# Kernel optimization log

Hardware: AMD Instinct MI355X
Metric: run time of the kernel (lower is better)

## Reference

```python
import jax, jax.numpy as jnp
import numpy as np

NL, DM, DS, DC, EX = 4, 1024, 16, 4, 2
DI = EX * DM          # 2048 inner dim
DTR = DM // 16        # 64 dt_rank
HID, OUT = 2048, 1000
B, L = 2, 1024
EPS = 1e-5

def _ln(x, w, b):
    m = jnp.mean(x, -1, keepdims=True)
    v = jnp.var(x, -1, keepdims=True)
    return (x - m) / jnp.sqrt(v + EPS) * w + b

def _silu(x):
    return x * jax.nn.sigmoid(x)

def _dwconv(x, w, b):
    # x: (B,L,C), w: (C,K) depthwise causal conv
    K = w.shape[1]
    xp = jnp.pad(x, ((0, 0), (K - 1, 0), (0, 0)))
    kern = jnp.transpose(w)[:, None, :]  # (K,1,C)
    y = jax.lax.conv_general_dilated(xp, kern, (1,), 'VALID',
                                     dimension_numbers=('NLC', 'LIO', 'NLC'),
                                     feature_group_count=x.shape[-1])
    return y + b

def _selective_scan(xs_, dt, Bm, Cm, A, Dv):
    # xs_, dt: (B,L,DI); Bm, Cm: (B,L,DS); A: (DI,DS); Dv: (DI,)
    def step(h, inp):
        x_t, dt_t, B_t, C_t = inp  # (B,DI),(B,DI),(B,DS),(B,DS)
        dA = jnp.exp(dt_t[..., None] * A)                       # (B,DI,DS)
        h = dA * h + dt_t[..., None] * B_t[:, None, :] * x_t[..., None]
        return h, jnp.einsum('bdn,bn->bd', h, C_t)
    h0 = jnp.zeros((xs_.shape[0], A.shape[0], A.shape[1]), xs_.dtype)
    seq = tuple(jnp.swapaxes(t, 0, 1) for t in (xs_, dt, Bm, Cm))
    _, ys = jax.lax.scan(step, h0, seq)
    return jnp.swapaxes(ys, 0, 1) + xs_ * Dv

def _mamba_block(x, ipw, cw, cb, xpw, dpw, dpb, Alog, Dv, opw):
    xz = jnp.einsum('bld,ed->ble', x, ipw)          # (B,L,2*DI)
    xs_, z = jnp.split(xz, 2, -1)
    xs_ = _silu(_dwconv(xs_, cw, cb))
    xdbl = jnp.einsum('bld,ed->ble', xs_, xpw)      # (B,L,DTR+2*DS)
    dt, Bm, Cm = jnp.split(xdbl, [DTR, DTR + DS], -1)
    dt = jax.nn.softplus(jnp.einsum('blr,dr->bld', dt, dpw) + dpb)
    A = -jnp.exp(Alog)
    y = _selective_scan(xs_, dt, Bm, Cm, A, Dv)
    y = y * _silu(z)
    return jnp.einsum('bld,ed->ble', y, opw)

def setup_inputs() -> dict:
    key = jax.random.key(0)
    ks = jax.random.split(key, 16)
    s = 0.02
    return {
        'x': jax.random.normal(ks[0], (B, L, DM), jnp.float32),
        'ln_w': jnp.ones((NL, DM)), 'ln_b': jnp.zeros((NL, DM)),
        'in_proj_w': jax.random.normal(ks[1], (NL, 2 * DI, DM)) * s,
        'conv_w': jax.random.normal(ks[2], (NL, DI, DC)) * s,
        'conv_b': jnp.zeros((NL, DI)),
        'x_proj_w': jax.random.normal(ks[3], (NL, DTR + 2 * DS, DI)) * s,
        'dt_proj_w': jax.random.normal(ks[4], (NL, DI, DTR)) * s,
        'dt_proj_b': jax.random.uniform(ks[5], (NL, DI), minval=-4.0, maxval=-2.0),
        'A_log': jnp.log(jnp.broadcast_to(jnp.arange(1, DS + 1, dtype=jnp.float32), (NL, DI, DS)) + 0.0),
        'Dv': jnp.ones((NL, DI)),
        'out_proj_w': jax.random.normal(ks[6], (NL, DM, DI)) * s,
        'fn_w': jnp.ones((DM,)), 'fn_b': jnp.zeros((DM,)),
        'h1_w': jax.random.normal(ks[7], (HID, DM)) * s, 'h1_b': jnp.zeros((HID,)),
        'hln_w': jnp.ones((HID,)), 'hln_b': jnp.zeros((HID,)),
        'h2_w': jax.random.normal(ks[8], (OUT, HID)) * s, 'h2_b': jnp.zeros((OUT,)),
    }

def reference(x, ln_w, ln_b, in_proj_w, conv_w, conv_b, x_proj_w, dt_proj_w,
              dt_proj_b, A_log, Dv, out_proj_w, fn_w, fn_b,
              h1_w, h1_b, hln_w, hln_b, h2_w, h2_b):
    for i in range(NL):
        res = x
        xn = _ln(x, ln_w[i], ln_b[i])
        x = _mamba_block(xn, in_proj_w[i], conv_w[i], conv_b[i], x_proj_w[i],
                         dt_proj_w[i], dt_proj_b[i], A_log[i], Dv[i], out_proj_w[i]) + res
    x = _ln(x, fn_w, fn_b)
    last = x[:, -1, :]                               # (B, DM)
    h = jax.nn.gelu(_ln(last @ h1_w.T + h1_b, hln_w, hln_b), approximate=False)
    return h @ h2_w.T + h2_b                         # (B, OUT)
```

## Files before the change

### kernel.cpp

```cpp
#include <hip/hip_runtime.h>

typedef unsigned short u16;
using short8 = __attribute__((ext_vector_type(8))) short;
using f32x4  = __attribute__((ext_vector_type(4))) float;

#define NLAYER 4
#define DMODEL 1024
#define DSTATE 16
#define DINNER 2048
#define DTRANK 64
#define SEQL   1024
#define NBATCH 2
#define MTOK   2048
#define NCH    64
#define CLEN   16
#define XPK    16

__device__ __forceinline__ u16 f2bf(float f) {
  union { float f; unsigned int u; } cv; cv.f = f;
  return (u16)((cv.u + 0x7FFFu + ((cv.u >> 16) & 1u)) >> 16);
}
__device__ __forceinline__ float bf2f(u16 v) {
  union { unsigned int u; float f; } cv; cv.u = ((unsigned int)v) << 16; return cv.f;
}

__global__ __launch_bounds__(256) void f32_to_bf16_l(const float* __restrict__ src,
                                                     u16* __restrict__ dst, int nper) {
  int l = blockIdx.y;
  int i4 = (blockIdx.x * 256 + threadIdx.x) * 4;
  if (i4 >= nper) return;
  float4 v = *(const float4*)&src[(size_t)l * nper + i4];
  ushort4 o; o.x = f2bf(v.x); o.y = f2bf(v.y); o.z = f2bf(v.z); o.w = f2bf(v.w);
  *(ushort4*)&dst[(size_t)l * nper + i4] = o;
}

__global__ __launch_bounds__(256) void cvt_pad_xproj_l(const float* __restrict__ src,
                                                       u16* __restrict__ dst) {
  int l = blockIdx.y;
  int i4 = (blockIdx.x * 256 + threadIdx.x) * 4;
  int row = i4 >> 11, col = i4 & 2047;
  float4 v = make_float4(0.f, 0.f, 0.f, 0.f);
  if (row < 96) v = *(const float4*)&src[(size_t)l * 96 * 2048 + row * 2048 + col];
  ushort4 o; o.x = f2bf(v.x); o.y = f2bf(v.y); o.z = f2bf(v.z); o.w = f2bf(v.w);
  *(ushort4*)&dst[(size_t)l * 128 * 2048 + i4] = o;
}

__global__ __launch_bounds__(256) void ln_to_bf16_k(const float* __restrict__ X,
    const float* __restrict__ w, const float* __restrict__ b, u16* __restrict__ out) {
  int row = blockIdx.x, tid = threadIdx.x;
  const float* x = X + (size_t)row * 1024;
  float4 v = ((const float4*)x)[tid];
  float s = v.x + v.y + v.z + v.w;
  float q = v.x*v.x + v.y*v.y + v.z*v.z + v.w*v.w;
  for (int o = 32; o; o >>= 1) { s += __shfl_down(s, o); q += __shfl_down(q, o); }
  __shared__ float sb[4], qb[4];
  int wv = tid >> 6, lane = tid & 63;
  if (lane == 0) { sb[wv] = s; qb[wv] = q; }
  __syncthreads();
  s = sb[0] + sb[1] + sb[2] + sb[3];
  q = qb[0] + qb[1] + qb[2] + qb[3];
  float mean = s * (1.f / 1024.f);
  float var  = q * (1.f / 1024.f) - mean * mean;
  float rstd = rsqrtf(var + 1e-5f);
  float4 wv4 = ((const float4*)w)[tid];
  float4 bv4 = ((const float4*)b)[tid];
  ushort4 o4;
  o4.x = f2bf((v.x - mean) * rstd * wv4.x + bv4.x);
  o4.y = f2bf((v.y - mean) * rstd * wv4.y + bv4.y);
  o4.z = f2bf((v.z - mean) * rstd * wv4.z + bv4.z);
  o4.w = f2bf((v.w - mean) * rstd * wv4.w + bv4.w);
  ((ushort4*)(out + (size_t)row * 1024))[tid] = o4;
}

__device__ __forceinline__ void stage_tile(const u16* G, int ld, int row0, int k0,
                                           u16* S, int tid) {
  int w = tid >> 6;
#pragma unroll
  for (int j = 0; j < 2; ++j) {
    int t = tid + j * 256;
    int r = t >> 2;
    int c = (t & 3) << 3;
    const u16* g = G + (size_t)(row0 + r) * ld + (k0 + c);
    u16* s = S + w * 512 + j * 2048;
    __builtin_amdgcn_global_load_lds((const __attribute__((address_space(1))) void*)g,
                                     (__attribute__((address_space(3))) void*)s,
                                     16, 0, 0);
  }
}
__device__ __forceinline__ void stage512(const u16* G, int ld, int row0, int k0,
                                         u16* S, int tid) {
  int r = tid >> 2;
  int c = (tid & 3) << 3;
  const u16* g = G + (size_t)(row0 + r) * ld + (k0 + c);
  u16* s = S + (tid >> 6) * 512;
  __builtin_amdgcn_global_load_lds((const __attribute__((address_space(1))) void*)g,
                                   (__attribute__((address_space(3))) void*)s,
                                   16, 0, 0);
}

template<int EPI, int SWZ>
__global__ __launch_bounds__(512) void gemm_bt(const u16* __restrict__ A,
    const u16* __restrict__ Bw, float* __restrict__ C,
    int lda, int ldb, int ldc, int kchunk, int nbm, int zstride) {
  __shared__ u16 As[2][128 * 32];
  __shared__ u16 Bs[2][128 * 32];
  int tid = threadIdx.x;
  int bm, bn;
  if (SWZ) {
    int l = blockIdx.x;
    int xcd = l & 7;
    int idx = l >> 3;
    int bnr = (int)(gridDim.x >> 3) / nbm;
    bm = idx % nbm;
    bn = xcd * bnr + idx / nbm;
  } else {
    bm = blockIdx.x; bn = blockIdx.y;
  }
  int kb = blockIdx.z * kchunk, ke = kb + kchunk;
  int lane = tid & 63;
  int w = tid >> 6;
  int wr = (w >> 2) * 64;
  int wc = (w & 3) * 32;
  int fr = lane & 15;
  int kg = (lane >> 4) * 8;
  f32x4 acc[4][2] = {};
  int cur = 0;
  stage512(A, lda, bm * 128, kb, As[0], tid);
  stage512(Bw, ldb, bn * 128, kb, Bs[0], tid);
  __syncthreads();
  for (int k0 = kb; k0 < ke; k0 += 32) {
    int kn = k0 + 32;
    if (kn < ke) {
      stage512(A, lda, bm * 128, kn, As[cur ^ 1], tid);
      stage512(Bw, ldb, bn * 128, kn, Bs[cur ^ 1], tid);
    }
    short8 a[4], b[2];
#pragma unroll
    for (int mf = 0; mf < 4; ++mf)
      a[mf] = *(const short8*)&As[cur][(wr + mf * 16 + fr) * 32 + kg];
#pragma unroll
    for (int nf = 0; nf < 2; ++nf)
      b[nf] = *(const short8*)&Bs[cur][(wc + nf * 16 + fr) * 32 + kg];
#pragma unroll
    for (int mf = 0; mf < 4; ++mf)
#pragma unroll
      for (int nf = 0; nf < 2; ++nf)
        acc[mf][nf] = __builtin_amdgcn_mfma_f32_16x16x32_bf16(a[mf], b[nf], acc[mf][nf], 0, 0, 0);
    __syncthreads();
    cur ^= 1;
  }
  int r0 = bm * 128 + wr + (lane >> 4) * 4;
  int c0 = bn * 128 + wc + fr;
  size_t zoff = (EPI == 0) ? (size_t)blockIdx.z * zstride : 0;
#pragma unroll
  for (int mf = 0; mf < 4; ++mf) {
#pragma unroll
    for (int nf = 0; nf < 2; ++nf) {
#pragma unroll
      for (int r = 0; r < 4; ++r) {
        int gr = r0 + mf * 16 + r;
        int gc = c0 + nf * 16;
        float v = acc[mf][nf][r];
        size_t idx = (size_t)gr * ldc + gc;
        if (EPI == 0) {
          C[zoff + idx] = v;
        } else if (EPI == 1) {
          ((u16*)C)[idx] = f2bf(v);
        } else {
          atomicAdd(&C[idx], v);
        }
      }
    }
  }
}

__global__ __launch_bounds__(256) void reduce_xdbl_k(const float* __restrict__ part,
                                                     float* __restrict__ xdbl_l) {
  int i4 = (blockIdx.x * 256 + threadIdx.x) * 4;
  float4 s = *(const float4*)&part[i4];
#pragma unroll
  for (int z = 1; z < XPK; ++z) {
    float4 v = *(const float4*)&part[(size_t)z * (MTOK * 128) + i4];
    s.x += v.x; s.y += v.y; s.z += v.z; s.w += v.w;
  }
  *(float4*)&xdbl_l[i4] = s;
}

__global__ __launch_bounds__(256) void conv_silu_k(const u16* __restrict__ xzb,
    const float* __restrict__ cw, const float* __restrict__ cb,
    u16* __restrict__ xsb) {
  int idx = blockIdx.x * 256 + threadIdx.x;
  int m = idx >> 8;
  int d = (idx & 255) << 3;
  int t = m & (SEQL - 1);
  float4 w4[8];
#pragma unroll
  for (int i = 0; i < 8; ++i) w4[i] = *(const float4*)&cw[(d + i) * 4];
  float acc[8];
#pragma unroll
  for (int q = 0; q < 2; ++q) {
    float4 c4 = *(const float4*)&cb[d + q * 4];
    acc[q*4+0] = c4.x; acc[q*4+1] = c4.y; acc[q*4+2] = c4.z; acc[q*4+3] = c4.w;
  }
#pragma unroll
  for (int j = 0; j < 4; ++j) {
    int tt = t - 3 + j;
    if (tt >= 0) {
      short8 xv = *(const short8*)&xzb[(size_t)(m - 3 + j) * 4096 + d];
#pragma unroll
      for (int i = 0; i < 8; ++i)
        acc[i] += bf2f((u16)xv[i]) * ((const float*)&w4[i])[j];
    }
  }
  short8 ob;
#pragma unroll
  for (int i = 0; i < 8; ++i) {
    float o = acc[i] / (1.f + __expf(-acc[i]));
    ob[i] = (short)f2bf(o);
  }
  *(short8*)&xsb[(size_t)m * 2048 + d] = ob;
}

__global__ __launch_bounds__(256) void gemm_dt_k(const float* __restrict__ Af,
    const u16* __restrict__ Bw, const float* __restrict__ bias, u16* __restrict__ Cout) {
  __shared__ u16 As[128 * 32];
  __shared__ u16 Bs[128 * 32];
  int tid = threadIdx.x;
  int bm = blockIdx.x, bn = blockIdx.y;
  int lane = tid & 63, w = tid >> 6;
  int wr = (w >> 1) * 64, wc = (w & 1) * 64;
  int fr = lane & 15;
  int kg = (lane >> 4) * 8;
  f32x4 acc[4][4] = {};
  int r  = tid >> 1;
  int cc = (tid & 1) * 16;
  for (int k0 = 0; k0 < 64; k0 += 32) {
    const float* src = &Af[(size_t)(bm * 128 + r) * 128 + k0 + cc];
    float4 f0 = *(const float4*)&src[0];
    float4 f1 = *(const float4*)&src[4];
    float4 f2 = *(const float4*)&src[8];
    float4 f3 = *(const float4*)&src[12];
    short8 o0, o1;
    o0[0]=(short)f2bf(f0.x); o0[1]=(short)f2bf(f0.y); o0[2]=(short)f2bf(f0.z); o0[3]=(short)f2bf(f0.w);
    o0[4]=(short)f2bf(f1.x); o0[5]=(short)f2bf(f1.y); o0[6]=(short)f2bf(f1.z); o0[7]=(short)f2bf(f1.w);
    o1[0]=(short)f2bf(f2.x); o1[1]=(short)f2bf(f2.y); o1[2]=(short)f2bf(f2.z); o1[3]=(short)f2bf(f2.w);
    o1[4]=(short)f2bf(f3.x); o1[5]=(short)f2bf(f3.y); o1[6]=(short)f2bf(f3.z); o1[7]=(short)f2bf(f3.w);
    __syncthreads();
    *(short8*)&As[r * 32 + cc]     = o0;
    *(short8*)&As[r * 32 + cc + 8] = o1;
    stage_tile(Bw, 64, bn * 128, k0, Bs, tid);
    __syncthreads();
    short8 a[4], b[4];
#pragma unroll
    for (int mf = 0; mf < 4; ++mf)
      a[mf] = *(const short8*)&As[(wr + mf * 16 + fr) * 32 + kg];
#pragma unroll
    for (int nf = 0; nf < 4; ++nf)
      b[nf] = *(const short8*)&Bs[(wc + nf * 16 + fr) * 32 + kg];
#pragma unroll
    for (int mf = 0; mf < 4; ++mf)
#pragma unroll
      for (int nf = 0; nf < 4; ++nf)
        acc[mf][nf] = __builtin_amdgcn_mfma_f32_16x16x32_bf16(a[mf], b[nf], acc[mf][nf], 0, 0, 0);
  }
  int r0 = bm * 128 + wr + (lane >> 4) * 4;
  int c0 = bn * 128 + wc + fr;
#pragma unroll
  for (int mf = 0; mf < 4; ++mf)
#pragma unroll
    for (int nf = 0; nf < 4; ++nf)
#pragma unroll
      for (int rr = 0; rr < 4; ++rr) {
        int gr = r0 + mf * 16 + rr;
        int gc = c0 + nf * 16;
        float v = acc[mf][nf][rr] + bias[gc];
        v = (v > 20.f) ? v : log1pf(__expf(v));
        Cout[(size_t)gr * 2048 + gc] = f2bf(v);
      }
}

__global__ __launch_bounds__(256) void scan_part1(const u16* __restrict__ dtb,
    const u16* __restrict__ xsb, const float* __restrict__ xdbl,
    const float* __restrict__ Alog, float* __restrict__ PS_S, float* __restrict__ sumdt_a) {
  int tid = threadIdx.x;
  int dg = blockIdx.x & 7;
  int ch = (blockIdx.x >> 3) & (NCH - 1);
  int b  = blockIdx.x >> 9;
  int d  = dg * 256 + tid;
  float Ar[16];
#pragma unroll
  for (int q = 0; q < 4; ++q) {
    float4 a = *(const float4*)&Alog[d * 16 + q * 4];
    Ar[q*4+0] = -__expf(a.x); Ar[q*4+1] = -__expf(a.y);
    Ar[q*4+2] = -__expf(a.z); Ar[q*4+3] = -__expf(a.w);
  }
  __shared__ float Bsh[CLEN][16];
  {
    int t = tid >> 4, n = tid & 15;
    int mm = b * SEQL + ch * CLEN + t;
    Bsh[t][n] = xdbl[mm * 128 + 64 + n];
  }
  __syncthreads();
  int mbase = b * SEQL + ch * CLEN;
  float dtv[CLEN], xv[CLEN];
#pragma unroll
  for (int t = 0; t < CLEN; ++t) dtv[t] = bf2f(dtb[(size_t)(mbase + t) * 2048 + d]);
#pragma unroll
  for (int t = 0; t < CLEN; ++t) xv[t] = bf2f(xsb[(size_t)(mbase + t) * 2048 + d]);
  float S[16];
#pragma unroll
  for (int n = 0; n < 16; ++n) S[n] = 0.f;
  float sumdt = 0.f;
  for (int t = 0; t < CLEN; ++t) {
    sumdt += dtv[t];
    float dx = dtv[t] * xv[t];
    float4 B0 = *(const float4*)&Bsh[t][0];
    float4 B1 = *(const float4*)&Bsh[t][4];
    float4 B2 = *(const float4*)&Bsh[t][8];
    float4 B3 = *(const float4*)&Bsh[t][12];
    const float* Bp[4] = {(const float*)&B0, (const float*)&B1, (const float*)&B2, (const float*)&B3};
#pragma unroll
    for (int n = 0; n < 16; ++n)
      S[n] = __expf(dtv[t] * Ar[n]) * S[n] + dx * Bp[n >> 2][n & 3];
  }
  size_t base = ((size_t)(b * NCH + ch) * 16) * 2048 + d;
#pragma unroll
  for (int n = 0; n < 16; ++n) PS_S[base + (size_t)n * 2048] = S[n];
  sumdt_a[(size_t)(b * NCH + ch) * 2048 + d] = sumdt;
}

__global__ __launch_bounds__(256) void scan_prefix(const float* __restrict__ PS_S,
    const float* __restrict__ sumdt_a, const float* __restrict__ Alog,
    u16* __restrict__ Hb) {
  int id = blockIdx.x * 256 + threadIdx.x;
  int d = id & 2047;
  int n = (id >> 11) & 15;
  int b = id >> 15;
  float Ar = -__expf(Alog[d * 16 + n]);
  size_t sbase = ((size_t)(b * NCH) * 16 + n) * 2048 + d;
  size_t dbase = (size_t)(b * NCH) * 2048 + d;
  float h = 0.f;
#pragma unroll 8
  for (int ch = 0; ch < NCH; ++ch) {
    Hb[sbase + (size_t)ch * (16 * 2048)] = f2bf(h);
    float S  = PS_S[sbase + (size_t)ch * (16 * 2048)];
    float sd = sumdt_a[dbase + (size_t)ch * 2048];
    h = fmaf(__expf(Ar * sd), h, S);
  }
}

__global__ __launch_bounds__(256) void scan_part2(const u16* __restrict__ dtb,
    const u16* __restrict__ xsb, const float* __restrict__ xdbl,
    const float* __restrict__ Alog, const float* __restrict__ Dv,
    const u16* __restrict__ xzb, const u16* __restrict__ Hb,
    u16* __restrict__ yg) {
  int tid = threadIdx.x;
  int dg = blockIdx.x & 7;
  int ch = (blockIdx.x >> 3) & (NCH - 1);
  int b  = blockIdx.x >> 9;
  int d  = dg * 256 + tid;
  float Ar[16];
#pragma unroll
  for (int q = 0; q < 4; ++q) {
    float4 a = *(const float4*)&Alog[d * 16 + q * 4];
    Ar[q*4+0] = -__expf(a.x); Ar[q*4+1] = -__expf(a.y);
    Ar[q*4+2] = -__expf(a.z); Ar[q*4+3] = -__expf(a.w);
  }
  float Dvd = Dv[d];
  __shared__ float BCs[CLEN][32];
  {
    int t = tid >> 5, n = tid & 31;
    int mm = b * SEQL + ch * CLEN + t;
    BCs[t][n] = xdbl[mm * 128 + 64 + n];
    BCs[t + 8][n] = xdbl[(mm + 8) * 128 + 64 + n];
  }
  size_t hbase = ((size_t)(b * NCH + ch) * 16) * 2048 + d;
  float h[16];
#pragma unroll
  for (int n = 0; n < 16; ++n) h[n] = bf2f(Hb[hbase + (size_t)n * 2048]);
  int mbase = b * SEQL + ch * CLEN;
  float dtv[CLEN], xv[CLEN], zv[CLEN];
#pragma unroll
  for (int t = 0; t < CLEN; ++t) dtv[t] = bf2f(dtb[(size_t)(mbase + t) * 2048 + d]);
#pragma unroll
  for (int t = 0; t < CLEN; ++t) xv[t] = bf2f(xsb[(size_t)(mbase + t) * 2048 + d]);
#pragma unroll
  for (int t = 0; t < CLEN; ++t) zv[t] = bf2f(xzb[(size_t)(mbase + t) * 4096 + 2048 + d]);
  __syncthreads();
  for (int t = 0; t < CLEN; ++t) {
    float dx = dtv[t] * xv[t];
    float4 B0 = *(const float4*)&BCs[t][0];
    float4 B1 = *(const float4*)&BCs[t][4];
    float4 B2 = *(const float4*)&BCs[t][8];
    float4 B3 = *(const float4*)&BCs[t][12];
    float4 C0 = *(const float4*)&BCs[t][16];
    float4 C1 = *(const float4*)&BCs[t][20];
    float4 C2 = *(const float4*)&BCs[t][24];
    float4 C3 = *(const float4*)&BCs[t][28];
    const float* Bp[4] = {(const float*)&B0, (const float*)&B1, (const float*)&B2, (const float*)&B3};
    const float* Cp[4] = {(const float*)&C0, (const float*)&C1, (const float*)&C2, (const float*)&C3};
#pragma unroll
    for (int n = 0; n < 16; ++n)
      h[n] = __expf(dtv[t] * Ar[n]) * h[n] + dx * Bp[n >> 2][n & 3];
    float y0 = 0.f, y1 = 0.f, y2 = 0.f, y3 = 0.f;
#pragma unroll
    for (int n = 0; n < 4; ++n) {
      y0 += h[n]      * Cp[0][n];
      y1 += h[4 + n]  * Cp[1][n];
      y2 += h[8 + n]  * Cp[2][n];
      y3 += h[12 + n] * Cp[3][n];
    }
    float y = (y0 + y1) + (y2 + y3) + xv[t] * Dvd;
    float sz = zv[t] / (1.f + __expf(-zv[t]));
    yg[(size_t)(mbase + t) * 2048 + d] = f2bf(y * sz);
  }
}

__global__ __launch_bounds__(256) void lnlast_gemv1_k(const float* __restrict__ xb,
    const float* __restrict__ fnw, const float* __restrict__ fnb,
    const float* __restrict__ h1w, const float* __restrict__ h1b,
    float* __restrict__ hpre) {
  int blk = blockIdx.x, tid = threadIdx.x;
  int b = blk >> 9;
  int jbase = (blk & 511) * 4;
  int wv = tid >> 6, lane = tid & 63;
  const float* x = xb + (size_t)(b * 1024 + 1023) * 1024;
  float4 v = ((const float4*)x)[tid];
  float s = v.x + v.y + v.z + v.w;
  float q = v.x*v.x + v.y*v.y + v.z*v.z + v.w*v.w;
  for (int o = 32; o; o >>= 1) { s += __shfl_down(s, o); q += __shfl_down(q, o); }
  __shared__ float sb[4], qb[4];
  __shared__ float row[1024];
  if (lane == 0) { sb[wv] = s; qb[wv] = q; }
  __syncthreads();
  s = sb[0] + sb[1] + sb[2] + sb[3];
  q = qb[0] + qb[1] + qb[2] + qb[3];
  float mean = s * (1.f / 1024.f);
  float rstd = rsqrtf(q * (1.f / 1024.f) - mean * mean + 1e-5f);
  float4 wv4 = ((const float4*)fnw)[tid];
  float4 bv4 = ((const float4*)fnb)[tid];
  float4 o;
  o.x = (v.x - mean) * rstd * wv4.x + bv4.x;
  o.y = (v.y - mean) * rstd * wv4.y + bv4.y;
  o.z = (v.z - mean) * rstd * wv4.z + bv4.z;
  o.w = (v.w - mean) * rstd * wv4.w + bv4.w;
  ((float4*)row)[tid] = o;
  __syncthreads();
  int j = jbase + wv;
  const float* w = h1w + (size_t)j * 1024;
  float acc = 0.f;
#pragma unroll
  for (int qq = 0; qq < 4; ++qq) {
    int col = qq * 256 + lane * 4;
    float4 xv = *(const float4*)&row[col];
    float4 wvv = *(const float4*)&w[col];
    acc += xv.x*wvv.x + xv.y*wvv.y + xv.z*wvv.z + xv.w*wvv.w;
  }
  for (int o2 = 32; o2; o2 >>= 1) acc += __shfl_down(acc, o2);
  if (lane == 0) hpre[b * 2048 + j] = acc + h1b[j];
}

__global__ __launch_bounds__(256) void lngelu_gemv2_k(const float* __restrict__ hpre,
    const float* __restrict__ hlnw, const float* __restrict__ hlnb,
    const float* __restrict__ h2w, const float* __restrict__ h2b,
    float* __restrict__ out) {
  int blk = blockIdx.x, tid = threadIdx.x;
  int b = (blk >= 250) ? 1 : 0;
  int jbase = (blk - b * 250) * 4;
  int wv = tid >> 6, lane = tid & 63;
  const float* x = hpre + b * 2048;
  float4 v0 = ((const float4*)x)[tid];
  float4 v1 = ((const float4*)x)[tid + 256];
  float s = v0.x+v0.y+v0.z+v0.w + v1.x+v1.y+v1.z+v1.w;
  float q = v0.x*v0.x+v0.y*v0.y+v0.z*v0.z+v0.w*v0.w
          + v1.x*v1.x+v1.y*v1.y+v1.z*v1.z+v1.w*v1.w;
  for (int o = 32; o; o >>= 1) { s += __shfl_down(s, o); q += __shfl_down(q, o); }
  __shared__ float sb[4], qb[4];
  __shared__ float row[2048];
  if (lane == 0) { sb[wv] = s; qb[wv] = q; }
  __syncthreads();
  s = sb[0] + sb[1] + sb[2] + sb[3];
  q = qb[0] + qb[1] + qb[2] + qb[3];
  float mean = s * (1.f / 2048.f);
  float rstd = rsqrtf(q * (1.f / 2048.f) - mean * mean + 1e-5f);
#pragma unroll
  for (int h = 0; h < 2; ++h) {
    float4 v = h ? v1 : v0;
    int c0 = tid * 4 + h * 1024;
    float4 wv4 = *(const float4*)&hlnw[c0];
    float4 bv4 = *(const float4*)&hlnb[c0];
    float4 g;
    g.x = (v.x - mean) * rstd * wv4.x + bv4.x;
    g.y = (v.y - mean) * rstd * wv4.y + bv4.y;
    g.z = (v.z - mean) * rstd * wv4.z + bv4.z;
    g.w = (v.w - mean) * rstd * wv4.w + bv4.w;
    g.x = 0.5f * g.x * (1.f + erff(g.x * 0.70710678f));
    g.y = 0.5f * g.y * (1.f + erff(g.y * 0.70710678f));
    g.z = 0.5f * g.z * (1.f + erff(g.z * 0.70710678f));
    g.w = 0.5f * g.w * (1.f + erff(g.w * 0.70710678f));
    *(float4*)&row[c0] = g;
  }
  __syncthreads();
  int j = jbase + wv;
  const float* w = h2w + (size_t)j * 2048;
  float acc = 0.f;
#pragma unroll
  for (int qq = 0; qq < 8; ++qq) {
    int col = qq * 256 + lane * 4;
    float4 xv = *(const float4*)&row[col];
    float4 wvv = *(const float4*)&w[col];
    acc += xv.x*wvv.x + xv.y*wvv.y + xv.z*wvv.z + xv.w*wvv.w;
  }
  for (int o2 = 32; o2; o2 >>= 1) acc += __shfl_down(acc, o2);
  if (lane == 0) out[b * 1000 + j] = acc + h2b[j];
}

extern "C" void kernel_launch(void* const* d_in, const int* in_sizes, int n_in,
                              void* d_out, int out_size, void* d_ws, size_t ws_size,
                              hipStream_t stream) {
  const float* x_in = (const float*)d_in[0];
  const float* lnw  = (const float*)d_in[1];
  const float* lnb  = (const float*)d_in[2];
  const float* ipw  = (const float*)d_in[3];
  const float* cw   = (const float*)d_in[4];
  const float* cb   = (const float*)d_in[5];
  const float* xpw  = (const float*)d_in[6];
  const float* dpw  = (const float*)d_in[7];
  const float* dpb  = (const float*)d_in[8];
  const float* Alog = (const float*)d_in[9];
  const float* Dv   = (const float*)d_in[10];
  const float* opw  = (const float*)d_in[11];
  const float* fnw  = (const float*)d_in[12];
  const float* fnb  = (const float*)d_in[13];
  const float* h1w  = (const float*)d_in[14];
  const float* h1b  = (const float*)d_in[15];
  const float* hlnw = (const float*)d_in[16];
  const float* hlnb = (const float*)d_in[17];
  const float* h2w  = (const float*)d_in[18];
  const float* h2b  = (const float*)d_in[19];
  float* out = (float*)d_out;

  char* ws = (char*)d_ws;
  size_t off = 0;
  auto alloc = [&](size_t bytes) -> void* {
    void* p = ws + off; off += (bytes + 255) & ~(size_t)255; return p;
  };
  float* x_buf   = (float*)alloc((size_t)MTOK * DMODEL * 4);
  u16*   xn_bf   = (u16*)  alloc((size_t)MTOK * DMODEL * 2);
  u16*   xz_bf   = (u16*)  alloc((size_t)MTOK * 2 * DINNER * 2);
  u16*   xs_bf   = (u16*)  alloc((size_t)MTOK * DINNER * 2);
  float* xpart   = (float*)alloc((size_t)XPK * MTOK * 128 * 4);
  float* xdbl_l  = (float*)alloc((size_t)MTOK * 128 * 4);
  u16*   dtb     = (u16*)  alloc((size_t)MTOK * DINNER * 2);
  u16*   yg_bf   = (u16*)  alloc((size_t)MTOK * DINNER * 2);
  u16*   w_ip4   = (u16*)  alloc((size_t)NLAYER * 2 * DINNER * DMODEL * 2);
  u16*   w_xp4   = (u16*)  alloc((size_t)NLAYER * 128 * DINNER * 2);
  u16*   w_dt4   = (u16*)  alloc((size_t)NLAYER * DINNER * DTRANK * 2);
  u16*   w_op4   = (u16*)  alloc((size_t)NLAYER * DMODEL * DINNER * 2);
  float* PS_S    = (float*)alloc((size_t)NBATCH * NCH * 16 * 2048 * 4);
  float* sumdt_a = (float*)alloc((size_t)NBATCH * NCH * 2048 * 4);
  u16*   Hb      = (u16*)  alloc((size_t)NBATCH * NCH * 16 * 2048 * 2);
  float* hpre    = (float*)alloc(2 * 2048 * 4);

  hipMemcpyAsync(x_buf, x_in, (size_t)MTOK * DMODEL * 4, hipMemcpyDeviceToDevice, stream);
  { dim3 g(4096, 4); f32_to_bf16_l<<<g, 256, 0, stream>>>(ipw, w_ip4, 2 * DINNER * DMODEL); }
  { dim3 g(256, 4);  cvt_pad_xproj_l<<<g, 256, 0, stream>>>(xpw, w_xp4); }
  { dim3 g(128, 4);  f32_to_bf16_l<<<g, 256, 0, stream>>>(dpw, w_dt4, DINNER * DTRANK); }
  { dim3 g(2048, 4); f32_to_bf16_l<<<g, 256, 0, stream>>>(opw, w_op4, DMODEL * DINNER); }

  for (int i = 0; i < NLAYER; ++i) {
    ln_to_bf16_k<<<MTOK, 256, 0, stream>>>(x_buf, lnw + i * DMODEL, lnb + i * DMODEL, xn_bf);
    gemm_bt<1, 1><<<dim3(512, 1, 1), 512, 0, stream>>>(
        xn_bf, w_ip4 + (size_t)i * 2 * DINNER * DMODEL, (float*)xz_bf,
        1024, 1024, 4096, 1024, 16, 0);
    conv_silu_k<<<2048, 256, 0, stream>>>(xz_bf, cw + (size_t)i * DINNER * 4, cb + i * DINNER, xs_bf);
    { dim3 g(16, 1, XPK);
      gemm_bt<0, 0><<<g, 512, 0, stream>>>(xs_bf, w_xp4 + (size_t)i * 128 * DINNER,
                                           xpart, 2048, 2048, 128, 128, 16, MTOK * 128); }
    reduce_xdbl_k<<<256, 256, 0, stream>>>(xpart, xdbl_l);
    { dim3 g(16, 16, 1);
      gemm_dt_k<<<g, 256, 0, stream>>>(xdbl_l, w_dt4 + (size_t)i * DINNER * DTRANK,
                                       dpb + i * DINNER, dtb); }
    scan_part1<<<1024, 256, 0, stream>>>(dtb, xs_bf, xdbl_l,
                                         Alog + (size_t)i * DINNER * DSTATE, PS_S, sumdt_a);
    scan_prefix<<<256, 256, 0, stream>>>(PS_S, sumdt_a, Alog + (size_t)i * DINNER * DSTATE, Hb);
    scan_part2<<<1024, 256, 0, stream>>>(dtb, xs_bf, xdbl_l, Alog + (size_t)i * DINNER * DSTATE,
                                         Dv + i * DINNER, xz_bf, Hb, yg_bf);
    gemm_bt<3, 1><<<dim3(128, 1, 2), 512, 0, stream>>>(
        yg_bf, w_op4 + (size_t)i * DMODEL * DINNER, x_buf,
        2048, 2048, 1024, 1024, 16, 0);
  }
  lnlast_gemv1_k<<<1024, 256, 0, stream>>>(x_buf, fnw, fnb, h1w, h1b, hpre);
  lngelu_gemv2_k<<<500, 256, 0, stream>>>(hpre, hlnw, hlnb, h2w, h2b, out);
  (void)in_sizes; (void)n_in; (void)out_size; (void)ws_size;
}
```

Before: 693.4 us.

## Fuse chunked scan stages into cooperative kernel and stage GEMM bf16 epilogue through LDS

Merges the three selective-scan kernels (chunk-local scan, inter-chunk prefix, final output pass) into a single cooperative kernel separated by grid-wide syncs. dt and x stay in registers across phases, and the prefix phase is split four ways per (d,n) with a small shared-memory combine, which shortens the serial chain over 64 chunks. Separately, the bf16 in_proj GEMM epilogue now writes through LDS so that global stores are coalesced 16-byte vectors. The cooperative launch needs all 1024 blocks to be co-resident and adds grid-barrier cost, and the prefix phase reads PS_S twice.

```diff
diff --git a/kernel.cpp b/kernel.cpp
--- a/kernel.cpp
+++ b/kernel.cpp
@@ -1,4 +1,6 @@
 #include <hip/hip_runtime.h>
+#include <hip/hip_cooperative_groups.h>
+namespace cg = cooperative_groups;
 
 typedef unsigned short u16;
 using short8 = __attribute__((ext_vector_type(8))) short;
@@ -102,8 +104,11 @@
 __global__ __launch_bounds__(512) void gemm_bt(const u16* __restrict__ A,
     const u16* __restrict__ Bw, float* __restrict__ C,
     int lda, int ldb, int ldc, int kchunk, int nbm, int zstride) {
-  __shared__ u16 As[2][128 * 32];
-  __shared__ u16 Bs[2][128 * 32];
+  __shared__ u16 SMEM[16384];
+  u16* As0 = SMEM;
+  u16* As1 = SMEM + 4096;
+  u16* Bs0 = SMEM + 8192;
+  u16* Bs1 = SMEM + 12288;
   int tid = threadIdx.x;
   int bm, bn;
   if (SWZ) {
@@ -125,22 +130,24 @@
   int kg = (lane >> 4) * 8;
   f32x4 acc[4][2] = {};
   int cur = 0;
-  stage512(A, lda, bm * 128, kb, As[0], tid);
-  stage512(Bw, ldb, bn * 128, kb, Bs[0], tid);
+  stage512(A, lda, bm * 128, kb, As0, tid);
+  stage512(Bw, ldb, bn * 128, kb, Bs0, tid);
   __syncthreads();
   for (int k0 = kb; k0 < ke; k0 += 32) {
     int kn = k0 + 32;
     if (kn < ke) {
-      stage512(A, lda, bm * 128, kn, As[cur ^ 1], tid);
-      stage512(Bw, ldb, bn * 128, kn, Bs[cur ^ 1], tid);
-    }
+      stage512(A, lda, bm * 128, kn, cur ? As0 : As1, tid);
+      stage512(Bw, ldb, bn * 128, kn, cur ? Bs0 : Bs1, tid);
+    }
+    const u16* Ac = cur ? As1 : As0;
+    const u16* Bc = cur ? Bs1 : Bs0;
     short8 a[4], b[2];
 #pragma unroll
     for (int mf = 0; mf < 4; ++mf)
-      a[mf] = *(const short8*)&As[cur][(wr + mf * 16 + fr) * 32 + kg];
+      a[mf] = *(const short8*)&Ac[(wr + mf * 16 + fr) * 32 + kg];
 #pragma unroll
     for (int nf = 0; nf < 2; ++nf)
-      b[nf] = *(const short8*)&Bs[cur][(wc + nf * 16 + fr) * 32 + kg];
+      b[nf] = *(const short8*)&Bc[(wc + nf * 16 + fr) * 32 + kg];
 #pragma unroll
     for (int mf = 0; mf < 4; ++mf)
 #pragma unroll
@@ -149,25 +156,43 @@
     __syncthreads();
     cur ^= 1;
   }
-  int r0 = bm * 128 + wr + (lane >> 4) * 4;
-  int c0 = bn * 128 + wc + fr;
-  size_t zoff = (EPI == 0) ? (size_t)blockIdx.z * zstride : 0;
-#pragma unroll
-  for (int mf = 0; mf < 4; ++mf) {
-#pragma unroll
-    for (int nf = 0; nf < 2; ++nf) {
-#pragma unroll
-      for (int r = 0; r < 4; ++r) {
-        int gr = r0 + mf * 16 + r;
-        int gc = c0 + nf * 16;
-        float v = acc[mf][nf][r];
-        size_t idx = (size_t)gr * ldc + gc;
-        if (EPI == 0) {
-          C[zoff + idx] = v;
-        } else if (EPI == 1) {
-          ((u16*)C)[idx] = f2bf(v);
-        } else {
-          atomicAdd(&C[idx], v);
+  if (EPI == 1) {
+#pragma unroll
+    for (int mf = 0; mf < 4; ++mf)
+#pragma unroll
+      for (int nf = 0; nf < 2; ++nf)
+#pragma unroll
+        for (int r = 0; r < 4; ++r) {
+          int lr = wr + (lane >> 4) * 4 + mf * 16 + r;
+          int lc = wc + fr + nf * 16;
+          SMEM[lr * 128 + lc] = f2bf(acc[mf][nf][r]);
+        }
+    __syncthreads();
+    int row = tid >> 2, c0l = (tid & 3) * 32;
+    u16* dst = (u16*)C + (size_t)(bm * 128 + row) * ldc + bn * 128 + c0l;
+    const u16* srcl = &SMEM[row * 128 + c0l];
+#pragma unroll
+    for (int s = 0; s < 4; ++s)
+      *(short8*)&dst[s * 8] = *(const short8*)&srcl[s * 8];
+  } else {
+    int r0 = bm * 128 + wr + (lane >> 4) * 4;
+    int c0 = bn * 128 + wc + fr;
+    size_t zoff = (EPI == 0) ? (size_t)blockIdx.z * zstride : 0;
+#pragma unroll
+    for (int mf = 0; mf < 4; ++mf) {
+#pragma unroll
+      for (int nf = 0; nf < 2; ++nf) {
+#pragma unroll
+        for (int r = 0; r < 4; ++r) {
+          int gr = r0 + mf * 16 + r;
+          int gc = c0 + nf * 16;
+          float v = acc[mf][nf][r];
+          size_t idx = (size_t)gr * ldc + gc;
+          if (EPI == 0) {
+            C[zoff + idx] = v;
+          } else {
+            atomicAdd(&C[idx], v);
+          }
         }
       }
     }
@@ -279,9 +304,13 @@
       }
 }
 
-__global__ __launch_bounds__(256) void scan_part1(const u16* __restrict__ dtb,
+__global__ __launch_bounds__(256) void scan_fused_k(const u16* __restrict__ dtb,
     const u16* __restrict__ xsb, const float* __restrict__ xdbl,
-    const float* __restrict__ Alog, float* __restrict__ PS_S, float* __restrict__ sumdt_a) {
+    const float* __restrict__ Alog, const float* __restrict__ Dv,
+    const u16* __restrict__ xzb, float* __restrict__ PS_S,
+    float* __restrict__ sumdt_a, u16* __restrict__ Hb, u16* __restrict__ yg) {
+  cg::grid_group grid = cg::this_grid();
+  __shared__ float smem[512];
   int tid = threadIdx.x;
   int dg = blockIdx.x & 7;
   int ch = (blockIdx.x >> 3) & (NCH - 1);
@@ -294,11 +323,10 @@
     Ar[q*4+0] = -__expf(a.x); Ar[q*4+1] = -__expf(a.y);
     Ar[q*4+2] = -__expf(a.z); Ar[q*4+3] = -__expf(a.w);
   }
-  __shared__ float Bsh[CLEN][16];
   {
     int t = tid >> 4, n = tid & 15;
     int mm = b * SEQL + ch * CLEN + t;
-    Bsh[t][n] = xdbl[mm * 128 + 64 + n];
+    smem[t * 16 + n] = xdbl[mm * 128 + 64 + n];
   }
   __syncthreads();
   int mbase = b * SEQL + ch * CLEN;
@@ -307,108 +335,88 @@
   for (int t = 0; t < CLEN; ++t) dtv[t] = bf2f(dtb[(size_t)(mbase + t) * 2048 + d]);
 #pragma unroll
   for (int t = 0; t < CLEN; ++t) xv[t] = bf2f(xsb[(size_t)(mbase + t) * 2048 + d]);
-  float S[16];
-#pragma unroll
-  for (int n = 0; n < 16; ++n) S[n] = 0.f;
-  float sumdt = 0.f;
-  for (int t = 0; t < CLEN; ++t) {
-    sumdt += dtv[t];
-    float dx = dtv[t] * xv[t];
-    float4 B0 = *(const float4*)&Bsh[t][0];
-    float4 B1 = *(const float4*)&Bsh[t][4];
-    float4 B2 = *(const float4*)&Bsh[t][8];
-    float4 B3 = *(const float4*)&Bsh[t][12];
-    const float* Bp[4] = {(const float*)&B0, (const float*)&B1, (const float*)&B2, (const float*)&B3};
-#pragma unroll
-    for (int n = 0; n < 16; ++n)
-      S[n] = __expf(dtv[t] * Ar[n]) * S[n] + dx * Bp[n >> 2][n & 3];
-  }
-  size_t base = ((size_t)(b * NCH + ch) * 16) * 2048 + d;
-#pragma unroll
-  for (int n = 0; n < 16; ++n) PS_S[base + (size_t)n * 2048] = S[n];
-  sumdt_a[(size_t)(b * NCH + ch) * 2048 + d] = sumdt;
-}
-
-__global__ __launch_bounds__(256) void scan_prefix(const float* __restrict__ PS_S,
-    const float* __restrict__ sumdt_a, const float* __restrict__ Alog,
-    u16* __restrict__ Hb) {
-  int id = blockIdx.x * 256 + threadIdx.x;
-  int d = id & 2047;
-  int n = (id >> 11) & 15;
-  int b = id >> 15;
-  float Ar = -__expf(Alog[d * 16 + n]);
-  size_t sbase = ((size_t)(b * NCH) * 16 + n) * 2048 + d;
-  size_t dbase = (size_t)(b * NCH) * 2048 + d;
-  float h = 0.f;
-#pragma unroll 8
-  for (int ch = 0; ch < NCH; ++ch) {
-    Hb[sbase + (size_t)ch * (16 * 2048)] = f2bf(h);
-    float S  = PS_S[sbase + (size_t)ch * (16 * 2048)];
-    float sd = sumdt_a[dbase + (size_t)ch * 2048];
-    h = fmaf(__expf(Ar * sd), h, S);
-  }
-}
-
-__global__ __launch_bounds__(256) void scan_part2(const u16* __restrict__ dtb,
-    const u16* __restrict__ xsb, const float* __restrict__ xdbl,
-    const float* __restrict__ Alog, const float* __restrict__ Dv,
-    const u16* __restrict__ xzb, const u16* __restrict__ Hb,
-    u16* __restrict__ yg) {
-  int tid = threadIdx.x;
-  int dg = blockIdx.x & 7;
-  int ch = (blockIdx.x >> 3) & (NCH - 1);
-  int b  = blockIdx.x >> 9;
-  int d  = dg * 256 + tid;
-  float Ar[16];
-#pragma unroll
-  for (int q = 0; q < 4; ++q) {
-    float4 a = *(const float4*)&Alog[d * 16 + q * 4];
-    Ar[q*4+0] = -__expf(a.x); Ar[q*4+1] = -__expf(a.y);
-    Ar[q*4+2] = -__expf(a.z); Ar[q*4+3] = -__expf(a.w);
-  }
-  float Dvd = Dv[d];
-  __shared__ float BCs[CLEN][32];
+  {
+    float S[16];
+#pragma unroll
+    for (int n = 0; n < 16; ++n) S[n] = 0.f;
+    float sumdt = 0.f;
+    for (int t = 0; t < CLEN; ++t) {
+      sumdt += dtv[t];
+      float dx = dtv[t] * xv[t];
+#pragma unroll
+      for (int n = 0; n < 16; ++n)
+        S[n] = __expf(dtv[t] * Ar[n]) * S[n] + dx * smem[t * 16 + n];
+    }
+    size_t base = ((size_t)(b * NCH + ch) * 16) * 2048 + d;
+#pragma unroll
+    for (int n = 0; n < 16; ++n) PS_S[base + (size_t)n * 2048] = S[n];
+    sumdt_a[(size_t)(b * NCH + ch) * 2048 + d] = sumdt;
+  }
+  __threadfence();
+  grid.sync();
+  {
+    int id = blockIdx.x * 256 + tid;
+    int q = id & 3;
+    int item = id >> 2;
+    int dd = item & 2047;
+    int n2 = (item >> 11) & 15;
+    int bb = item >> 15;
+    float Arn = -__expf(Alog[dd * 16 + n2]);
+    size_t sb = ((size_t)(bb * NCH) * 16 + n2) * 2048 + dd;
+    size_t db = (size_t)(bb * NCH) * 2048 + dd;
+    float Pl = 1.f, Sl = 0.f;
+#pragma unroll
+    for (int j = 0; j < 16; ++j) {
+      int c2 = q * 16 + j;
+      float Sv = PS_S[sb + (size_t)c2 * 32768];
+      float Pv = __expf(Arn * sumdt_a[db + (size_t)c2 * 2048]);
+      Sl = Pv * Sl + Sv;
+      Pl = Pv * Pl;
+    }
+    smem[tid] = Pl; smem[256 + tid] = Sl;
+    __syncthreads();
+    int g = tid & ~3;
+    float h = 0.f;
+    for (int j = 0; j < q; ++j) h = smem[g + j] * h + smem[256 + g + j];
+#pragma unroll
+    for (int j = 0; j < 16; ++j) {
+      int c2 = q * 16 + j;
+      Hb[sb + (size_t)c2 * 32768] = f2bf(h);
+      float Sv = PS_S[sb + (size_t)c2 * 32768];
+      float Pv = __expf(Arn * sumdt_a[db + (size_t)c2 * 2048]);
+      h = Pv * h + Sv;
+    }
+  }
+  __threadfence();
+  grid.sync();
+  __syncthreads();
   {
     int t = tid >> 5, n = tid & 31;
     int mm = b * SEQL + ch * CLEN + t;
-    BCs[t][n] = xdbl[mm * 128 + 64 + n];
-    BCs[t + 8][n] = xdbl[(mm + 8) * 128 + 64 + n];
-  }
+    smem[t * 32 + n] = xdbl[mm * 128 + 64 + n];
+    smem[(t + 8) * 32 + n] = xdbl[(mm + 8) * 128 + 64 + n];
+  }
+  float Dvd = Dv[d];
   size_t hbase = ((size_t)(b * NCH + ch) * 16) * 2048 + d;
   float h[16];
 #pragma unroll
   for (int n = 0; n < 16; ++n) h[n] = bf2f(Hb[hbase + (size_t)n * 2048]);
-  int mbase = b * SEQL + ch * CLEN;
-  float dtv[CLEN], xv[CLEN], zv[CLEN];
-#pragma unroll
-  for (int t = 0; t < CLEN; ++t) dtv[t] = bf2f(dtb[(size_t)(mbase + t) * 2048 + d]);
-#pragma unroll
-  for (int t = 0; t < CLEN; ++t) xv[t] = bf2f(xsb[(size_t)(mbase + t) * 2048 + d]);
+  float zv[CLEN];
 #pragma unroll
   for (int t = 0; t < CLEN; ++t) zv[t] = bf2f(xzb[(size_t)(mbase + t) * 4096 + 2048 + d]);
   __syncthreads();
   for (int t = 0; t < CLEN; ++t) {
     float dx = dtv[t] * xv[t];
-    float4 B0 = *(const float4*)&BCs[t][0];
-    float4 B1 = *(const float4*)&BCs[t][4];
-    float4 B2 = *(const float4*)&BCs[t][8];
-    float4 B3 = *(const float4*)&BCs[t][12];
-    float4 C0 = *(const float4*)&BCs[t][16];
-    float4 C1 = *(const float4*)&BCs[t][20];
-    float4 C2 = *(const float4*)&BCs[t][24];
-    float4 C3 = *(const float4*)&BCs[t][28];
-    const float* Bp[4] = {(const float*)&B0, (const float*)&B1, (const float*)&B2, (const float*)&B3};
-    const float* Cp[4] = {(const float*)&C0, (const float*)&C1, (const float*)&C2, (const float*)&C3};
 #pragma unroll
     for (int n = 0; n < 16; ++n)
-      h[n] = __expf(dtv[t] * Ar[n]) * h[n] + dx * Bp[n >> 2][n & 3];
+      h[n] = __expf(dtv[t] * Ar[n]) * h[n] + dx * smem[t * 32 + n];
     float y0 = 0.f, y1 = 0.f, y2 = 0.f, y3 = 0.f;
 #pragma unroll
     for (int n = 0; n < 4; ++n) {
-      y0 += h[n]      * Cp[0][n];
-      y1 += h[4 + n]  * Cp[1][n];
-      y2 += h[8 + n]  * Cp[2][n];
-      y3 += h[12 + n] * Cp[3][n];
+      y0 += h[n]      * smem[t * 32 + 16 + n];
+      y1 += h[4 + n]  * smem[t * 32 + 20 + n];
+      y2 += h[8 + n]  * smem[t * 32 + 24 + n];
+      y3 += h[12 + n] * smem[t * 32 + 28 + n];
     }
     float y = (y0 + y1) + (y2 + y3) + xv[t] * Dvd;
     float sz = zv[t] / (1.f + __expf(-zv[t]));
@@ -581,11 +589,21 @@
     { dim3 g(16, 16, 1);
       gemm_dt_k<<<g, 256, 0, stream>>>(xdbl_l, w_dt4 + (size_t)i * DINNER * DTRANK,
                                        dpb + i * DINNER, dtb); }
-    scan_part1<<<1024, 256, 0, stream>>>(dtb, xs_bf, xdbl_l,
-                                         Alog + (size_t)i * DINNER * DSTATE, PS_S, sumdt_a);
-    scan_prefix<<<256, 256, 0, stream>>>(PS_S, sumdt_a, Alog + (size_t)i * DINNER * DSTATE, Hb);
-    scan_part2<<<1024, 256, 0, stream>>>(dtb, xs_bf, xdbl_l, Alog + (size_t)i * DINNER * DSTATE,
-                                         Dv + i * DINNER, xz_bf, Hb, yg_bf);
+    {
+      const u16*   a0 = dtb;
+      const u16*   a1 = xs_bf;
+      const float* a2 = xdbl_l;
+      const float* a3 = Alog + (size_t)i * DINNER * DSTATE;
+      const float* a4 = Dv + (size_t)i * DINNER;
+      const u16*   a5 = xz_bf;
+      float*       a6 = PS_S;
+      float*       a7 = sumdt_a;
+      u16*         a8 = Hb;
+      u16*         a9 = yg_bf;
+      void* kargs[10] = {&a0, &a1, &a2, &a3, &a4, &a5, &a6, &a7, &a8, &a9};
+      hipLaunchCooperativeKernel((const void*)scan_fused_k, dim3(1024), dim3(256),
+                                 kargs, 0, stream);
+    }
     gemm_bt<3, 1><<<dim3(128, 1, 2), 512, 0, stream>>>(
         yg_bf, w_op4 + (size_t)i * DMODEL * DINNER, x_buf,
         2048, 2048, 1024, 1024, 16, 0);
```

Result: slower. 2.290 ms (+230.3%).
